# Optimization experiments

Hardware: AMD Instinct MI355X
Metric: run time of the kernel (lower is better)

Reference implementation:

```python
import jax, jax.numpy as jnp
import numpy as np


def setup_inputs() -> dict:
    key = jax.random.key(0)
    k1, k2 = jax.random.split(key)
    B, C, h, w = 8, 128, 56, 56
    query_feature = jax.random.normal(k1, (B, C, h, w), dtype=jnp.float32)
    support_feature = jax.random.normal(k2, (B, C, h, w), dtype=jnp.float32)
    return {"query_feature": query_feature, "support_feature": support_feature}


def reference(query_feature, support_feature):
    q, s = query_feature, support_feature
    B, C, h, w = support_feature.shape
    N = h * w
    # torch .view semantics == row-major reshape (NOT a transpose)
    qf = jnp.reshape(query_feature, (B, N, C))      # [B, N, C]
    sf = jnp.reshape(support_feature, (B, C, N))    # [B, C, N]
    batch_adj = jnp.einsum('bnc,bcm->bnm', qf, sf)  # [B, N, N]
    attn = jax.nn.softmax(batch_adj, axis=-1)
    query_logits = jnp.einsum('bnm,bmc->bnc', attn, qf)          # [B, N, C]
    attention_mask = jax.nn.sigmoid(jnp.sum(batch_adj, axis=-1)) # [B, N]
    query_logits = query_logits * attention_mask[..., None]
    sf2 = jnp.reshape(support_feature, (B, N, C))   # another raw view
    support_logits = sf2 * attention_mask[..., None]
    query_logits = jnp.reshape(query_logits, (B, C, h, w))
    support_logits = jnp.reshape(support_logits, (B, C, h, w))
    return (q + query_logits, s + support_logits)
```

## Files before the change

kernel.cpp:

```cpp
#include <hip/hip_runtime.h>
#include <math.h>

#define B_ 8
#define C_ 128
#define N_ 3136
#define MT 64
#define TILES 49
#define QTBIG 128
#define QTILES 25

typedef short bf16x8 __attribute__((ext_vector_type(8)));
typedef float f32x4 __attribute__((ext_vector_type(4)));

__device__ __forceinline__ unsigned short f2bf(float f) {
    union { float f; unsigned u; } x; x.f = f;
    return (unsigned short)((x.u + 0x8000u) >> 16);
}

__device__ __forceinline__ void gl_lds16(const void* g, void* l) {
    __builtin_amdgcn_global_load_lds(
        (const __attribute__((address_space(1))) unsigned int*)g,
        (__attribute__((address_space(3))) unsigned int*)l, 16, 0, 0);
}

__global__ __launch_bounds__(256) void colsum_kernel(const float* __restrict__ s,
                                                     float* __restrict__ csum) {
    int blk = blockIdx.x;
    const float* p = s + (size_t)blk * N_;
    float acc = 0.f;
    for (int i = threadIdx.x; i < N_; i += 256) acc += p[i];
#pragma unroll
    for (int off = 32; off > 0; off >>= 1) acc += __shfl_down(acc, off, 64);
    __shared__ float part[4];
    if ((threadIdx.x & 63) == 0) part[threadIdx.x >> 6] = acc;
    __syncthreads();
    if (threadIdx.x == 0) csum[blk] = part[0] + part[1] + part[2] + part[3];
}

__global__ __launch_bounds__(256) void prep_kernel(const float* __restrict__ q,
                                                   const float* __restrict__ s,
                                                   unsigned short* __restrict__ sfT,
                                                   unsigned short* __restrict__ qfT,
                                                   float* __restrict__ csum) {
    __shared__ unsigned short T[8448];
    const int tid = threadIdx.x, bid = blockIdx.x;
    const int b = bid & 7, m0 = (bid >> 3) * 64;
    const float* sb = s + (size_t)b * C_ * N_;
    const float* qb = q + (size_t)b * C_ * N_;

    unsigned short (*TA)[132] = (unsigned short (*)[132])T;
#pragma unroll
    for (int st = 0; st < 8; ++st) {
        int idx = st * 256 + tid;
        int c = idx >> 4, m4 = (idx & 15) * 4;
        float4 v = *(const float4*)&sb[(size_t)c * N_ + m0 + m4];
        TA[m4 + 0][c] = f2bf(v.x);
        TA[m4 + 1][c] = f2bf(v.y);
        TA[m4 + 2][c] = f2bf(v.z);
        TA[m4 + 3][c] = f2bf(v.w);
        float ps = (v.x + v.y) + (v.z + v.w);
        ps += __shfl_xor(ps, 1, 16);
        ps += __shfl_xor(ps, 2, 16);
        ps += __shfl_xor(ps, 4, 16);
        ps += __shfl_xor(ps, 8, 16);
        if ((tid & 15) == 0) atomicAdd(&csum[b * C_ + c], ps);
    }
    __syncthreads();
    {
        unsigned short* dst = sfT + (size_t)b * N_ * C_;
#pragma unroll
        for (int st = 0; st < 4; ++st) {
            int g = st * 256 + tid;
            int mr = g >> 4, p = g & 15;
            int sw = (mr & 15) ^ ((mr >> 1) & 4);
            int lch = p ^ sw;
            const unsigned short* src = &TA[mr][lch * 8];
            ushort4 a = *(const ushort4*)src;
            ushort4 bq = *(const ushort4*)(src + 4);
            uint4 w;
            w.x = a.x | ((unsigned)a.y << 16);   w.y = a.z | ((unsigned)a.w << 16);
            w.z = bq.x | ((unsigned)bq.y << 16); w.w = bq.z | ((unsigned)bq.w << 16);
            *(uint4*)&dst[(size_t)(m0 + mr) * C_ + p * 8] = w;
        }
    }
    __syncthreads();

    unsigned short (*TB)[66] = (unsigned short (*)[66])T;
#pragma unroll
    for (int st = 0; st < 8; ++st) {
        int idx = st * 256 + tid;
        int r = idx >> 5, c4 = (idx & 31) * 4;
        float4 v = *(const float4*)&qb[(size_t)(m0 + r) * C_ + c4];
        TB[c4 + 0][r] = f2bf(v.x);
        TB[c4 + 1][r] = f2bf(v.y);
        TB[c4 + 2][r] = f2bf(v.z);
        TB[c4 + 3][r] = f2bf(v.w);
    }
    __syncthreads();
    {
        unsigned short* dstb = qfT + (size_t)b * N_ * C_;
#pragma unroll
        for (int st = 0; st < 4; ++st) {
            int g = st * 256 + tid;
            int p = g >> 7, c = g & 127;
            const unsigned short* src = &TB[c][p * 8];
            ushort2 a0 = *(const ushort2*)(src);
            ushort2 a1 = *(const ushort2*)(src + 2);
            ushort2 a2 = *(const ushort2*)(src + 4);
            ushort2 a3 = *(const ushort2*)(src + 6);
            uint4 w;
            w.x = a0.x | ((unsigned)a0.y << 16); w.y = a1.x | ((unsigned)a1.y << 16);
            w.z = a2.x | ((unsigned)a2.y << 16); w.w = a3.x | ((unsigned)a3.y << 16);
            *(uint4*)&dstb[((size_t)(m0 >> 6) * 8 + p) * (C_ * 8) + c * 8] = w;
        }
    }
}

__global__ __launch_bounds__(512, 1) void fused_full_kernel(
    const float* __restrict__ q, const float* __restrict__ s,
    const float* __restrict__ csum,
    const unsigned short* __restrict__ sfT,
    const unsigned short* __restrict__ qfT,
    float* __restrict__ out0, float* __restrict__ out1) {

    __shared__ __align__(16) unsigned char SM[QTBIG * 132 * 4];
    __shared__ float dred[2][QTBIG];
    __shared__ float mskd[QTBIG];
    __shared__ float cs[C_];

    unsigned short* Kb = (unsigned short*)SM;
    unsigned short* Vb = (unsigned short*)(SM + 32768);
    float (*Of)[132] = (float (*)[132])SM;

    const int tid = threadIdx.x;
    const int lane = tid & 63;
    const int wave = tid >> 6;
    const int l15 = lane & 15;
    const int quad = lane >> 4;
    const int qs = wave >> 1;
    const int mg = wave & 1;
    const int bid = blockIdx.x;
    const int b = bid & 7;
    const int qt = bid >> 3;
    const int n0 = qt * QTBIG;

    const float* qb = q + (size_t)b * C_ * N_;
    const unsigned short* sfTb = sfT + (size_t)b * N_ * C_;
    const unsigned short* qfTb = qfT + (size_t)b * N_ * C_;

    const int sig_base = ((l15 >> 2) << 3) + (l15 & 3);

    if (tid < C_) cs[tid] = csum[b * C_ + tid];

#pragma unroll
    for (int st = 0; st < 2; ++st) {
        int i = st * 512 + tid;
        gl_lds16(sfTb + (size_t)(i >> 4) * C_ + (i & 15) * 8,
                 &Kb[(st * 512 + wave * 64) * 8]);
        gl_lds16(qfTb + (size_t)i * 8,
                 &Vb[(st * 512 + wave * 64) * 8]);
    }
    __syncthreads();

    bf16x8 qa[2][4];
    float dotp[2];
#pragma unroll
    for (int rt = 0; rt < 2; ++rt) {
        int grow = n0 + qs * 32 + rt * 16 + l15;
        if (grow > N_ - 1) grow = N_ - 1;
        float dp = 0.f;
#pragma unroll
        for (int ks = 0; ks < 4; ++ks) {
            int c0 = ks * 32 + quad * 8;
            float4 f0 = *(const float4*)&qb[(size_t)grow * C_ + c0];
            float4 f1 = *(const float4*)&qb[(size_t)grow * C_ + c0 + 4];
            dp += f0.x * cs[c0 + 0] + f0.y * cs[c0 + 1] +
                  f0.z * cs[c0 + 2] + f0.w * cs[c0 + 3] +
                  f1.x * cs[c0 + 4] + f1.y * cs[c0 + 5] +
                  f1.z * cs[c0 + 6] + f1.w * cs[c0 + 7];
            union { unsigned short u[8]; bf16x8 v; } t;
            t.u[0] = f2bf(f0.x); t.u[1] = f2bf(f0.y);
            t.u[2] = f2bf(f0.z); t.u[3] = f2bf(f0.w);
            t.u[4] = f2bf(f1.x); t.u[5] = f2bf(f1.y);
            t.u[6] = f2bf(f1.z); t.u[7] = f2bf(f1.w);
            qa[rt][ks] = t.v;
        }
        dotp[rt] = dp;
    }
#pragma unroll
    for (int rt = 0; rt < 2; ++rt) {
        float d = dotp[rt];
        d += __shfl_xor(d, 16, 64);
        d += __shfl_xor(d, 32, 64);
        if (mg == 0 && quad == 0) mskd[qs * 32 + rt * 16 + l15] = d;
    }

    f32x4 O[2][8];
#pragma unroll
    for (int rt = 0; rt < 2; ++rt)
#pragma unroll
        for (int nt = 0; nt < 8; ++nt) O[rt][nt] = (f32x4){0.f, 0.f, 0.f, 0.f};
    float dsum[2] = {0.f, 0.f};

    for (int tt = 0; tt < TILES; ++tt) {
        const int cur = tt & 1;
        __syncthreads();

        if (tt + 1 < TILES) {
            const int nxt = cur ^ 1;
            const size_t m1 = (size_t)(tt + 1) * MT;
#pragma unroll
            for (int st = 0; st < 2; ++st) {
                int i = st * 512 + tid;
                gl_lds16(sfTb + (m1 + (i >> 4)) * C_ + (i & 15) * 8,
                         &Kb[nxt * (MT * C_) + (st * 512 + wave * 64) * 8]);
                gl_lds16(qfTb + (size_t)(tt + 1) * (MT * C_) + (size_t)i * 8,
                         &Vb[nxt * (MT * C_) + (st * 512 + wave * 64) * 8]);
            }
        }

        f32x4 acc[2][2];
        __builtin_amdgcn_s_setprio(1);
#pragma unroll
        for (int ct = 0; ct < 2; ++ct) {
            const int mrow = sig_base + (ct << 2);
            const int sw = (mrow & 15) ^ ((mrow >> 1) & 4);
            const int row = mg * 32 + mrow;
            acc[ct][0] = (f32x4){0.f, 0.f, 0.f, 0.f};
            acc[ct][1] = (f32x4){0.f, 0.f, 0.f, 0.f};
#pragma unroll
            for (int ks = 0; ks < 4; ++ks) {
                int ch = (ks * 4 + quad) ^ sw;
                bf16x8 af = *(const bf16x8*)&Kb[cur * (MT * C_) + row * C_ + ch * 8];
                acc[ct][0] = __builtin_amdgcn_mfma_f32_16x16x32_bf16(af, qa[0][ks], acc[ct][0], 0, 0, 0);
                acc[ct][1] = __builtin_amdgcn_mfma_f32_16x16x32_bf16(af, qa[1][ks], acc[ct][1], 0, 0, 0);
            }
        }
        __builtin_amdgcn_s_setprio(0);

        bf16x8 pa[2];
#pragma unroll
        for (int rt = 0; rt < 2; ++rt) {
            float e0 = __expf(acc[0][rt][0]);
            float e1 = __expf(acc[0][rt][1]);
            float e2 = __expf(acc[0][rt][2]);
            float e3 = __expf(acc[0][rt][3]);
            float e4 = __expf(acc[1][rt][0]);
            float e5 = __expf(acc[1][rt][1]);
            float e6 = __expf(acc[1][rt][2]);
            float e7 = __expf(acc[1][rt][3]);
            dsum[rt] += ((e0 + e1) + (e2 + e3)) + ((e4 + e5) + (e6 + e7));
            union { unsigned short u[8]; bf16x8 v; } pk;
            pk.u[0] = f2bf(e0); pk.u[1] = f2bf(e1);
            pk.u[2] = f2bf(e2); pk.u[3] = f2bf(e3);
            pk.u[4] = f2bf(e4); pk.u[5] = f2bf(e5);
            pk.u[6] = f2bf(e6); pk.u[7] = f2bf(e7);
            pa[rt] = pk.v;
        }

        __builtin_amdgcn_s_setprio(1);
#pragma unroll
        for (int nt = 0; nt < 8; ++nt) {
            bf16x8 vf = *(const bf16x8*)&Vb[cur * (MT * C_) + ((mg * 4 + quad) * C_ + nt * 16 + l15) * 8];
            O[0][nt] = __builtin_amdgcn_mfma_f32_16x16x32_bf16(pa[0], vf, O[0][nt], 0, 0, 0);
            O[1][nt] = __builtin_amdgcn_mfma_f32_16x16x32_bf16(pa[1], vf, O[1][nt], 0, 0, 0);
        }
        __builtin_amdgcn_s_setprio(0);
    }

#pragma unroll
    for (int rt = 0; rt < 2; ++rt) {
        float d = dsum[rt];
        d += __shfl_xor(d, 16, 64);
        d += __shfl_xor(d, 32, 64);
        if (quad == 0) dred[mg][qs * 32 + rt * 16 + l15] = d;
    }

    __syncthreads();

    if (mg == 1) {
#pragma unroll
        for (int rt = 0; rt < 2; ++rt)
#pragma unroll
            for (int nt = 0; nt < 8; ++nt)
#pragma unroll
                for (int r = 0; r < 4; ++r)
                    Of[qs * 32 + rt * 16 + quad * 4 + r][nt * 16 + l15] = O[rt][nt][r];
    }
    __syncthreads();
    if (mg == 0) {
#pragma unroll
        for (int rt = 0; rt < 2; ++rt)
#pragma unroll
            for (int nt = 0; nt < 8; ++nt)
#pragma unroll
                for (int r = 0; r < 4; ++r)
                    Of[qs * 32 + rt * 16 + quad * 4 + r][nt * 16 + l15] += O[rt][nt][r];
    }
    __syncthreads();

    const size_t vbase = (size_t)b * N_ * C_ + (size_t)n0 * C_;
#pragma unroll
    for (int it = 0; it < 8; ++it) {
        int row = it * 16 + (tid >> 5);
        int grow = n0 + row;
        if (grow >= N_) continue;
        int c = (tid & 31) * 4;
        float dt = dred[0][row] + dred[1][row];
        float mk = 1.0f / (1.0f + __expf(-mskd[row]));
        float scl = mk / dt;
        float om = 1.0f + mk;
        float4 o4 = *(const float4*)&Of[row][c];
        float4 q4 = *(const float4*)&q[vbase + (size_t)row * C_ + c];
        float4 s4 = *(const float4*)&s[vbase + (size_t)row * C_ + c];
        float4 r0v, r1v;
        r0v.x = q4.x + o4.x * scl;
        r0v.y = q4.y + o4.y * scl;
        r0v.z = q4.z + o4.z * scl;
        r0v.w = q4.w + o4.w * scl;
        r1v.x = s4.x * om; r1v.y = s4.y * om;
        r1v.z = s4.z * om; r1v.w = s4.w * om;
        *(float4*)&out0[vbase + (size_t)row * C_ + c] = r0v;
        *(float4*)&out1[vbase + (size_t)row * C_ + c] = r1v;
    }
}

__global__ __launch_bounds__(256, 2) void fused_kernel(const float* __restrict__ q,
                                                       const float* __restrict__ s,
                                                       const float* __restrict__ csum,
                                                       float* __restrict__ out0,
                                                       float* __restrict__ out1) {
    __shared__ float QtT[C_][68];
    __shared__ float Kt[C_ * 32];
    __shared__ float Vt[32 * C_];
    __shared__ float PT[32][68];
    __shared__ float mask_l[64];
    __shared__ float csum_l[C_];

    const int t = threadIdx.x;
    const int l = t & 63, w = t >> 6, tx = t & 15, ty = t >> 4;
    const int bid = blockIdx.x, b = bid & 7, n0 = (bid >> 3) * 64;
    const float* qb = q + (size_t)b * C_ * N_;
    const float* sb = s + (size_t)b * C_ * N_;

#pragma unroll
    for (int jj = 0; jj < 2; ++jj) {
        int c = l + 64 * jj;
#pragma unroll
        for (int i = 0; i < 16; ++i) QtT[c][w + 4 * i] = qb[(size_t)(n0 + w + 4 * i) * C_ + c];
    }
    if (t < C_) csum_l[t] = csum[b * C_ + t];
    __syncthreads();
    if (t < 64) {
        float d = 0.f;
        for (int c = 0; c < C_; ++c) d += QtT[c][t] * csum_l[c];
        mask_l[t] = 1.0f / (1.0f + __expf(-d));
    }
    float4 Oa[4], Ob[4];
#pragma unroll
    for (int i = 0; i < 4; ++i) { Oa[i] = make_float4(0,0,0,0); Ob[i] = make_float4(0,0,0,0); }
    float m_r[4], l_r[4];
#pragma unroll
    for (int i = 0; i < 4; ++i) { m_r[i] = -3.0e38f; l_r[i] = 0.f; }

    for (int mt = 0; mt < N_ / 32; ++mt) {
        const int m0 = mt * 32;
        __syncthreads();
#pragma unroll
        for (int i = 0; i < 4; ++i) {
            int s4 = (w * 4 + i) * 64 + l;
            int c = s4 >> 3, mq = (s4 & 7) * 4;
            *(float4*)&Kt[c * 32 + mq] = *(const float4*)&sb[(size_t)c * N_ + m0 + mq];
            *(float4*)&Vt[s4 * 4] = *(const float4*)&qb[(size_t)m0 * C_ + s4 * 4];
        }
        __syncthreads();
        float a[4][2];
#pragma unroll
        for (int i = 0; i < 4; ++i) a[i][0] = a[i][1] = 0.f;
#pragma unroll 4
        for (int k = 0; k < C_; ++k) {
            const float4 qv = *(const float4*)&QtT[k][4 * ty];
            const float2 kv = *(const float2*)&Kt[k * 32 + 2 * tx];
            a[0][0] = fmaf(qv.x, kv.x, a[0][0]); a[0][1] = fmaf(qv.x, kv.y, a[0][1]);
            a[1][0] = fmaf(qv.y, kv.x, a[1][0]); a[1][1] = fmaf(qv.y, kv.y, a[1][1]);
            a[2][0] = fmaf(qv.z, kv.x, a[2][0]); a[2][1] = fmaf(qv.z, kv.y, a[2][1]);
            a[3][0] = fmaf(qv.w, kv.x, a[3][0]); a[3][1] = fmaf(qv.w, kv.y, a[3][1]);
        }
#pragma unroll
        for (int i = 0; i < 4; ++i) {
            float tm = fmaxf(a[i][0], a[i][1]);
            tm = fmaxf(tm, __shfl_xor(tm, 1, 64)); tm = fmaxf(tm, __shfl_xor(tm, 2, 64));
            tm = fmaxf(tm, __shfl_xor(tm, 4, 64)); tm = fmaxf(tm, __shfl_xor(tm, 8, 64));
            float nm = fmaxf(m_r[i], tm);
            float al = __expf(m_r[i] - nm);
            m_r[i] = nm;
            float p0 = __expf(a[i][0] - nm), p1 = __expf(a[i][1] - nm);
            float ts = p0 + p1;
            ts += __shfl_xor(ts, 1, 64); ts += __shfl_xor(ts, 2, 64);
            ts += __shfl_xor(ts, 4, 64); ts += __shfl_xor(ts, 8, 64);
            l_r[i] = l_r[i] * al + ts;
            PT[2 * tx + 0][4 * ty + i] = p0;
            PT[2 * tx + 1][4 * ty + i] = p1;
            Oa[i].x *= al; Oa[i].y *= al; Oa[i].z *= al; Oa[i].w *= al;
            Ob[i].x *= al; Ob[i].y *= al; Ob[i].z *= al; Ob[i].w *= al;
        }
        __syncthreads();
#pragma unroll 2
        for (int j = 0; j < 32; ++j) {
            const float4 pv = *(const float4*)&PT[j][4 * ty];
            const float4 v0 = *(const float4*)&Vt[j * C_ + 4 * tx];
            const float4 v1 = *(const float4*)&Vt[j * C_ + 4 * tx + 64];
            Oa[0].x = fmaf(pv.x, v0.x, Oa[0].x); Oa[0].y = fmaf(pv.x, v0.y, Oa[0].y);
            Oa[0].z = fmaf(pv.x, v0.z, Oa[0].z); Oa[0].w = fmaf(pv.x, v0.w, Oa[0].w);
            Ob[0].x = fmaf(pv.x, v1.x, Ob[0].x); Ob[0].y = fmaf(pv.x, v1.y, Ob[0].y);
            Ob[0].z = fmaf(pv.x, v1.z, Ob[0].z); Ob[0].w = fmaf(pv.x, v1.w, Ob[0].w);
            Oa[1].x = fmaf(pv.y, v0.x, Oa[1].x); Oa[1].y = fmaf(pv.y, v0.y, Oa[1].y);
            Oa[1].z = fmaf(pv.y, v0.z, Oa[1].z); Oa[1].w = fmaf(pv.y, v0.w, Oa[1].w);
            Ob[1].x = fmaf(pv.y, v1.x, Ob[1].x); Ob[1].y = fmaf(pv.y, v1.y, Ob[1].y);
            Ob[1].z = fmaf(pv.y, v1.z, Ob[1].z); Ob[1].w = fmaf(pv.y, v1.w, Ob[1].w);
            Oa[2].x = fmaf(pv.z, v0.x, Oa[2].x); Oa[2].y = fmaf(pv.z, v0.y, Oa[2].y);
            Oa[2].z = fmaf(pv.z, v0.z, Oa[2].z); Oa[2].w = fmaf(pv.z, v0.w, Oa[2].w);
            Ob[2].x = fmaf(pv.z, v1.x, Ob[2].x); Ob[2].y = fmaf(pv.z, v1.y, Ob[2].y);
            Ob[2].z = fmaf(pv.z, v1.z, Ob[2].z); Ob[2].w = fmaf(pv.z, v1.w, Ob[2].w);
            Oa[3].x = fmaf(pv.w, v0.x, Oa[3].x); Oa[3].y = fmaf(pv.w, v0.y, Oa[3].y);
            Oa[3].z = fmaf(pv.w, v0.z, Oa[3].z); Oa[3].w = fmaf(pv.w, v0.w, Oa[3].w);
            Ob[3].x = fmaf(pv.w, v1.x, Ob[3].x); Ob[3].y = fmaf(pv.w, v1.y, Ob[3].y);
            Ob[3].z = fmaf(pv.w, v1.z, Ob[3].z); Ob[3].w = fmaf(pv.w, v1.w, Ob[3].w);
        }
    }
#pragma unroll
    for (int i = 0; i < 4; ++i) {
        const int r = 4 * ty + i;
        const float mk = mask_l[r];
        const float scl = mk / l_r[i];
        const float om = 1.0f + mk;
        const size_t row = (size_t)b * C_ * N_ + (size_t)(n0 + r) * C_;
#pragma unroll
        for (int h = 0; h < 2; ++h) {
            const int c = 4 * tx + 64 * h;
            const float4 ov = h ? Ob[i] : Oa[i];
            float4 qv = *(const float4*)&qb[(size_t)(n0 + r) * C_ + c];
            float4 sv = *(const float4*)&sb[(size_t)(n0 + r) * C_ + c];
            float4 o0, o1;
            o0.x = qv.x + ov.x * scl; o0.y = qv.y + ov.y * scl;
            o0.z = qv.z + ov.z * scl; o0.w = qv.w + ov.w * scl;
            o1.x = sv.x * om; o1.y = sv.y * om; o1.z = sv.z * om; o1.w = sv.w * om;
            *(float4*)&out0[row + c] = o0;
            *(float4*)&out1[row + c] = o1;
        }
    }
}

extern "C" void kernel_launch(void* const* d_in, const int* in_sizes, int n_in,
                              void* d_out, int out_size, void* d_ws, size_t ws_size,
                              hipStream_t stream) {
    const float* q = (const float*)d_in[0];
    const float* s = (const float*)d_in[1];
    float* out0 = (float*)d_out;
    float* out1 = out0 + (size_t)B_ * C_ * N_;
    float* csum = (float*)d_ws;

    const size_t elems = (size_t)B_ * N_ * C_;
    const size_t need = 4096
                      + 2 * elems * sizeof(unsigned short);

    if (ws_size >= need) {
        unsigned short* sfT = (unsigned short*)((char*)d_ws + 4096);
        unsigned short* qfT = sfT + elems;
        hipMemsetAsync(csum, 0, B_ * C_ * sizeof(float), stream);
        prep_kernel<<<B_ * TILES, 256, 0, stream>>>(q, s, sfT, qfT, csum);
        fused_full_kernel<<<QTILES * B_, 512, 0, stream>>>(q, s, csum, sfT, qfT, out0, out1);
    } else {
        colsum_kernel<<<B_ * C_, 256, 0, stream>>>(s, csum);
        fused_kernel<<<B_ * (N_ / 64), 256, 0, stream>>>(q, s, csum, out0, out1);
    }
}
```

Before: 162.2 us.

## Read K/V tiles directly from global memory and replace atomic colsum with partials

Removes the double-buffered global-to-LDS staging of the K and V bf16 tiles (and its per-tile barrier and XOR swizzle), so MFMA operands are now loaded straight from global memory and rely on the caches. It also replaces the memset plus atomicAdd column-sum with per-slice partial sums written to the workspace and summed by the fused kernel, which drops a memset launch and the atomic traffic. The risk is higher global/L2 latency on every MFMA operand load with no explicit prefetch, and the operand access pattern is no longer shaped for LDS. A 49-step reduction is added at the start of each fused block.

```diff
diff --git a/kernel.cpp b/kernel.cpp
--- a/kernel.cpp
+++ b/kernel.cpp
@@ -17,12 +17,6 @@
     return (unsigned short)((x.u + 0x8000u) >> 16);
 }
 
-__device__ __forceinline__ void gl_lds16(const void* g, void* l) {
-    __builtin_amdgcn_global_load_lds(
-        (const __attribute__((address_space(1))) unsigned int*)g,
-        (__attribute__((address_space(3))) unsigned int*)l, 16, 0, 0);
-}
-
 __global__ __launch_bounds__(256) void colsum_kernel(const float* __restrict__ s,
                                                      float* __restrict__ csum) {
     int blk = blockIdx.x;
@@ -41,10 +35,11 @@
                                                    const float* __restrict__ s,
                                                    unsigned short* __restrict__ sfT,
                                                    unsigned short* __restrict__ qfT,
-                                                   float* __restrict__ csum) {
+                                                   float* __restrict__ csump) {
     __shared__ unsigned short T[8448];
     const int tid = threadIdx.x, bid = blockIdx.x;
     const int b = bid & 7, m0 = (bid >> 3) * 64;
+    const int slice = bid >> 3;
     const float* sb = s + (size_t)b * C_ * N_;
     const float* qb = q + (size_t)b * C_ * N_;
 
@@ -63,7 +58,7 @@
         ps += __shfl_xor(ps, 2, 16);
         ps += __shfl_xor(ps, 4, 16);
         ps += __shfl_xor(ps, 8, 16);
-        if ((tid & 15) == 0) atomicAdd(&csum[b * C_ + c], ps);
+        if ((tid & 15) == 0) csump[((size_t)slice * 8 + b) * C_ + c] = ps;
     }
     __syncthreads();
     {
@@ -72,9 +67,7 @@
         for (int st = 0; st < 4; ++st) {
             int g = st * 256 + tid;
             int mr = g >> 4, p = g & 15;
-            int sw = (mr & 15) ^ ((mr >> 1) & 4);
-            int lch = p ^ sw;
-            const unsigned short* src = &TA[mr][lch * 8];
+            const unsigned short* src = &TA[mr][p * 8];
             ushort4 a = *(const ushort4*)src;
             ushort4 bq = *(const ushort4*)(src + 4);
             uint4 w;
@@ -118,19 +111,15 @@
 
 __global__ __launch_bounds__(512, 1) void fused_full_kernel(
     const float* __restrict__ q, const float* __restrict__ s,
-    const float* __restrict__ csum,
+    const float* __restrict__ csump,
     const unsigned short* __restrict__ sfT,
     const unsigned short* __restrict__ qfT,
     float* __restrict__ out0, float* __restrict__ out1) {
 
-    __shared__ __align__(16) unsigned char SM[QTBIG * 132 * 4];
+    __shared__ __align__(16) float Of[QTBIG][132];
     __shared__ float dred[2][QTBIG];
     __shared__ float mskd[QTBIG];
     __shared__ float cs[C_];
-
-    unsigned short* Kb = (unsigned short*)SM;
-    unsigned short* Vb = (unsigned short*)(SM + 32768);
-    float (*Of)[132] = (float (*)[132])SM;
 
     const int tid = threadIdx.x;
     const int lane = tid & 63;
@@ -150,15 +139,12 @@
 
     const int sig_base = ((l15 >> 2) << 3) + (l15 & 3);
 
-    if (tid < C_) cs[tid] = csum[b * C_ + tid];
-
-#pragma unroll
-    for (int st = 0; st < 2; ++st) {
-        int i = st * 512 + tid;
-        gl_lds16(sfTb + (size_t)(i >> 4) * C_ + (i & 15) * 8,
-                 &Kb[(st * 512 + wave * 64) * 8]);
-        gl_lds16(qfTb + (size_t)i * 8,
-                 &Vb[(st * 512 + wave * 64) * 8]);
+    if (tid < C_) {
+        float a = 0.f;
+#pragma unroll 7
+        for (int sl = 0; sl < TILES; ++sl)
+            a += csump[((size_t)sl * 8 + b) * C_ + tid];
+        cs[tid] = a;
     }
     __syncthreads();
 
@@ -203,35 +189,20 @@
     float dsum[2] = {0.f, 0.f};
 
     for (int tt = 0; tt < TILES; ++tt) {
-        const int cur = tt & 1;
-        __syncthreads();
-
-        if (tt + 1 < TILES) {
-            const int nxt = cur ^ 1;
-            const size_t m1 = (size_t)(tt + 1) * MT;
-#pragma unroll
-            for (int st = 0; st < 2; ++st) {
-                int i = st * 512 + tid;
-                gl_lds16(sfTb + (m1 + (i >> 4)) * C_ + (i & 15) * 8,
-                         &Kb[nxt * (MT * C_) + (st * 512 + wave * 64) * 8]);
-                gl_lds16(qfTb + (size_t)(tt + 1) * (MT * C_) + (size_t)i * 8,
-                         &Vb[nxt * (MT * C_) + (st * 512 + wave * 64) * 8]);
-            }
-        }
+        const unsigned short* Kt = sfTb + (size_t)tt * (MT * C_);
+        const unsigned short* Vt = qfTb + (size_t)tt * (MT * C_);
 
         f32x4 acc[2][2];
         __builtin_amdgcn_s_setprio(1);
 #pragma unroll
         for (int ct = 0; ct < 2; ++ct) {
             const int mrow = sig_base + (ct << 2);
-            const int sw = (mrow & 15) ^ ((mrow >> 1) & 4);
             const int row = mg * 32 + mrow;
             acc[ct][0] = (f32x4){0.f, 0.f, 0.f, 0.f};
             acc[ct][1] = (f32x4){0.f, 0.f, 0.f, 0.f};
 #pragma unroll
             for (int ks = 0; ks < 4; ++ks) {
-                int ch = (ks * 4 + quad) ^ sw;
-                bf16x8 af = *(const bf16x8*)&Kb[cur * (MT * C_) + row * C_ + ch * 8];
+                bf16x8 af = *(const bf16x8*)&Kt[(size_t)row * C_ + (ks * 4 + quad) * 8];
                 acc[ct][0] = __builtin_amdgcn_mfma_f32_16x16x32_bf16(af, qa[0][ks], acc[ct][0], 0, 0, 0);
                 acc[ct][1] = __builtin_amdgcn_mfma_f32_16x16x32_bf16(af, qa[1][ks], acc[ct][1], 0, 0, 0);
             }
@@ -261,7 +232,7 @@
         __builtin_amdgcn_s_setprio(1);
 #pragma unroll
         for (int nt = 0; nt < 8; ++nt) {
-            bf16x8 vf = *(const bf16x8*)&Vb[cur * (MT * C_) + ((mg * 4 + quad) * C_ + nt * 16 + l15) * 8];
+            bf16x8 vf = *(const bf16x8*)&Vt[((mg * 4 + quad) * C_ + nt * 16 + l15) * 8];
             O[0][nt] = __builtin_amdgcn_mfma_f32_16x16x32_bf16(pa[0], vf, O[0][nt], 0, 0, 0);
             O[1][nt] = __builtin_amdgcn_mfma_f32_16x16x32_bf16(pa[1], vf, O[1][nt], 0, 0, 0);
         }
@@ -275,8 +246,6 @@
         d += __shfl_xor(d, 32, 64);
         if (quad == 0) dred[mg][qs * 32 + rt * 16 + l15] = d;
     }
-
-    __syncthreads();
 
     if (mg == 1) {
 #pragma unroll
@@ -458,19 +427,20 @@
     const float* s = (const float*)d_in[1];
     float* out0 = (float*)d_out;
     float* out1 = out0 + (size_t)B_ * C_ * N_;
-    float* csum = (float*)d_ws;
 
     const size_t elems = (size_t)B_ * N_ * C_;
-    const size_t need = 4096
+    const size_t csump_sz = (size_t)TILES * B_ * C_;
+    const size_t need = csump_sz * sizeof(float)
                       + 2 * elems * sizeof(unsigned short);
 
     if (ws_size >= need) {
-        unsigned short* sfT = (unsigned short*)((char*)d_ws + 4096);
+        float* csump = (float*)d_ws;
+        unsigned short* sfT = (unsigned short*)(csump + csump_sz);
         unsigned short* qfT = sfT + elems;
-        hipMemsetAsync(csum, 0, B_ * C_ * sizeof(float), stream);
-        prep_kernel<<<B_ * TILES, 256, 0, stream>>>(q, s, sfT, qfT, csum);
-        fused_full_kernel<<<QTILES * B_, 512, 0, stream>>>(q, s, csum, sfT, qfT, out0, out1);
+        prep_kernel<<<B_ * TILES, 256, 0, stream>>>(q, s, sfT, qfT, csump);
+        fused_full_kernel<<<QTILES * B_, 512, 0, stream>>>(q, s, csump, sfT, qfT, out0, out1);
     } else {
+        float* csum = (float*)d_ws;
         colsum_kernel<<<B_ * C_, 256, 0, stream>>>(s, csum);
         fused_kernel<<<B_ * (N_ / 64), 256, 0, stream>>>(q, s, csum, out0, out1);
     }
```

Measured after the change: 272.5 us. 68.1% more time.
